# Optimization experiments

Hardware: AMD Instinct MI355X
Metric: run time of the kernel (lower is better)

Reference implementation:

```python
import jax, jax.numpy as jnp
import numpy as np


def _maxpool2x2(t):
    # t: [B, H, W, C] -> [B, H//2, W//2, C], 2x2 max pool stride 2
    B, H, W, C = t.shape
    return t.reshape(B, H // 2, 2, W // 2, 2, C).max(axis=(2, 4))


def setup_inputs() -> dict:
    key = jax.random.key(0)
    ks = jax.random.split(key, 7)
    B, H, W, C = 16, 64, 64, 256
    x = jax.random.normal(ks[0], (B, H, W, C), jnp.float32)
    w_theta = jax.random.normal(ks[1], (C, C // 8), jnp.float32) * 0.05
    w_phi = jax.random.normal(ks[2], (C, C // 8), jnp.float32) * 0.05
    w_g = jax.random.normal(ks[3], (C, C // 2), jnp.float32) * 0.05
    w_o = jax.random.normal(ks[4], (C // 2, C), jnp.float32) * 0.05
    b_o = jnp.zeros((C,), jnp.float32)
    sigma = jax.random.normal(ks[5], (), jnp.float32)
    return {"x": x, "w_theta": w_theta, "w_phi": w_phi, "w_g": w_g,
            "w_o": w_o, "b_o": b_o, "sigma": sigma}


def reference(x, w_theta, w_phi, w_g, w_o, b_o, sigma):
    B, H, W, C = x.shape
    L = H * W          # location_num = 4096
    Ld = L // 4        # downsampled_num (after 2x2 maxpool)
    # 1x1 convs == channel GEMMs
    theta = jnp.einsum('bhwc,cd->bhwd', x, w_theta).reshape(B, L, C // 8)
    phi = jnp.einsum('bhwc,cd->bhwd', x, w_phi)
    phi = _maxpool2x2(phi).reshape(B, Ld, C // 8)
    attn = jax.nn.softmax(jnp.einsum('bld,bmd->blm', theta, phi), axis=-1)  # [B, L, Ld]
    g = jnp.einsum('bhwc,cd->bhwd', x, w_g)
    g = _maxpool2x2(g).reshape(B, Ld, C // 2)
    attn_g = jnp.einsum('blm,bmd->bld', attn, g).reshape(B, H, W, C // 2)
    attn_g = jnp.einsum('bhwd,dc->bhwc', attn_g, w_o) + b_o
    return x + sigma * attn_g
```

## Files before the change

### kernel.cpp

```cpp
#include <hip/hip_runtime.h>
#include <hip/hip_bf16.h>


typedef __attribute__((ext_vector_type(8))) short bf16x8;
typedef __attribute__((ext_vector_type(4))) float f32x4;

#define MFMA16(A,B,C) __builtin_amdgcn_mfma_f32_16x16x32_bf16(A,B,C,0,0,0)

#define GLOAD16(GSRC, LDST)                                                        \
    __builtin_amdgcn_global_load_lds(                                              \
        (const __attribute__((address_space(1))) unsigned int*)(GSRC),             \
        (__attribute__((address_space(3))) unsigned int*)(LDST), 16, 0, 0)

static __device__ __forceinline__ unsigned short f2b(float f) {
    __hip_bfloat16 h = __float2bfloat16(f);
    return *reinterpret_cast<unsigned short*>(&h);
}
static __device__ __forceinline__ float blo(unsigned int u){ return __uint_as_float(u << 16); }
static __device__ __forceinline__ float bhi(unsigned int u){ return __uint_as_float(u & 0xffff0000u); }

__global__ void k_prep(const float* __restrict__ w_theta, const float* __restrict__ w_phi,
                       const float* __restrict__ w_g, const float* __restrict__ w_o,
                       unsigned short* __restrict__ WT, unsigned short* __restrict__ woT)
{
    int bid = blockIdx.x, t = threadIdx.x;
    if (bid < 192) {
        int n = bid;
        float v;
        if (n < 32)      v = w_theta[t * 32 + n];
        else if (n < 64) v = w_phi[t * 32 + (n - 32)];
        else             v = w_g[t * 128 + (n - 64)];
        WT[n * 256 + t] = f2b(v);
    } else if (t < 128) {
        int cc = bid - 192;
        woT[cc * 128 + t] = f2b(w_o[t * 256 + cc]);
    }
}

__global__ __launch_bounds__(256) void k_proj(
    const float* __restrict__ x, const unsigned short* __restrict__ WT,
    unsigned short* __restrict__ theta_b, unsigned short* __restrict__ phi_b,
    unsigned short* __restrict__ g_b)
{
    __shared__ unsigned short xT[128 * 64];
    __shared__ unsigned short wT[192 * 64];
    const int t = threadIdx.x;
    const int w = t >> 6, l = t & 63, G = l >> 4, c = l & 15;
    const size_t row0 = (size_t)blockIdx.x * 128;

    f32x4 acc[2][12];
#pragma unroll
    for (int i = 0; i < 2; i++)
#pragma unroll
        for (int j = 0; j < 12; j++) acc[i][j] = (f32x4){0.f, 0.f, 0.f, 0.f};

    for (int k0 = 0; k0 < 256; k0 += 64) {
        __syncthreads();
#pragma unroll
        for (int it = 0; it < 4; it++) {
            int u = it * 256 + t, r = u >> 3, s = u & 7;
            const float* px = x + (row0 + r) * 256 + k0 + s * 8;
            float4 a = *(const float4*)px;
            float4 bq = *(const float4*)(px + 4);
            uint4 v;
            v.x = (unsigned)f2b(a.x) | ((unsigned)f2b(a.y) << 16);
            v.y = (unsigned)f2b(a.z) | ((unsigned)f2b(a.w) << 16);
            v.z = (unsigned)f2b(bq.x) | ((unsigned)f2b(bq.y) << 16);
            v.w = (unsigned)f2b(bq.z) | ((unsigned)f2b(bq.w) << 16);
            *(uint4*)((char*)xT + r * 128 + ((s * 16) ^ ((r & 7) << 4))) = v;
        }
#pragma unroll
        for (int it = 0; it < 6; it++) {
            int u = it * 256 + t, r = u >> 3, s = u & 7;
            uint4 v = *(const uint4*)(WT + r * 256 + k0 + s * 8);
            *(uint4*)((char*)wT + r * 128 + ((s * 16) ^ ((r & 7) << 4))) = v;
        }
        __syncthreads();
#pragma unroll
        for (int kin = 0; kin < 2; kin++) {
            int m0r = (2 * w) * 16 + c, m1r = (2 * w + 1) * 16 + c;
            bf16x8 a0 = *(const bf16x8*)((char*)xT + m0r * 128 + ((kin * 64 + G * 16) ^ ((m0r & 7) << 4)));
            bf16x8 a1 = *(const bf16x8*)((char*)xT + m1r * 128 + ((kin * 64 + G * 16) ^ ((m1r & 7) << 4)));
#pragma unroll
            for (int nt = 0; nt < 12; nt++) {
                int nr = nt * 16 + c;
                bf16x8 bv = *(const bf16x8*)((char*)wT + nr * 128 + ((kin * 64 + G * 16) ^ ((nr & 7) << 4)));
                acc[0][nt] = MFMA16(a0, bv, acc[0][nt]);
                acc[1][nt] = MFMA16(a1, bv, acc[1][nt]);
            }
        }
    }
#pragma unroll
    for (int mt = 0; mt < 2; mt++)
#pragma unroll
        for (int nt = 0; nt < 12; nt++)
#pragma unroll
            for (int i = 0; i < 4; i++) {
                size_t row = row0 + (2 * w + mt) * 16 + 4 * G + i;
                unsigned short v = f2b(acc[mt][nt][i]);
                if (nt < 2)      theta_b[row * 32 + nt * 16 + c] = v;
                else if (nt < 4) phi_b[row * 32 + (nt - 2) * 16 + c] = v;
                else             g_b[row * 128 + (nt - 4) * 16 + c] = v;
            }
}

__global__ __launch_bounds__(256) void k_pool(
    const unsigned short* __restrict__ phi_b, const unsigned short* __restrict__ g_b,
    unsigned short* __restrict__ phi_p, unsigned short* __restrict__ g_pT)
{
    const int bid = blockIdx.x, t = threadIdx.x;
    if (bid < 1024) {
        const unsigned int* p32 = (const unsigned int*)phi_b;
        unsigned int* pp32 = (unsigned int*)phi_p;
        int idx = bid * 256 + t;
        int b = idx >> 14, r = idx & 16383, pm = r >> 4, d2 = r & 15;
        int hp = pm >> 5, wp = pm & 31;
        size_t base = ((size_t)b * 4096 + (2 * hp) * 64 + 2 * wp) * 16 + d2;
        unsigned v0 = p32[base], v1 = p32[base + 16], v2 = p32[base + 1024], v3 = p32[base + 1040];
        float lo = fmaxf(fmaxf(blo(v0), blo(v1)), fmaxf(blo(v2), blo(v3)));
        float hi = fmaxf(fmaxf(bhi(v0), bhi(v1)), fmaxf(bhi(v2), bhi(v3)));
        pp32[idx] = (unsigned)f2b(lo) | ((unsigned)f2b(hi) << 16);
    } else {
        __shared__ unsigned short P[32 * 128];
        int b = (bid - 1024) >> 5, hp = (bid - 1024) & 31;
        const unsigned int* g32 = (const unsigned int*)g_b;
#pragma unroll
        for (int it = 0; it < 8; it++) {
            int u = it * 256 + t, wp = u >> 6, d2 = u & 63;
            size_t base = ((size_t)b * 4096 + (2 * hp) * 64 + 2 * wp) * 64 + d2;
            unsigned v0 = g32[base], v1 = g32[base + 64], v2 = g32[base + 4096], v3 = g32[base + 4160];
            float lo = fmaxf(fmaxf(blo(v0), blo(v1)), fmaxf(blo(v2), blo(v3)));
            float hi = fmaxf(fmaxf(bhi(v0), bhi(v1)), fmaxf(bhi(v2), bhi(v3)));
            unsigned pv = (unsigned)f2b(lo) | ((unsigned)f2b(hi) << 16);
            *(unsigned*)((char*)P + wp * 256 + ((d2 * 4) ^ ((wp & 7) << 4))) = pv;
        }
        __syncthreads();
#pragma unroll
        for (int it = 0; it < 2; it++) {
            int d = t & 127, s4 = (t >> 7) + it * 2;
            union { unsigned short v[8]; uint4 q; } pk;
#pragma unroll
            for (int k = 0; k < 8; k++) {
                int wp = 16 * (k >> 2) + 4 * s4 + (k & 3);
                pk.v[k] = *(const unsigned short*)((char*)P + wp * 256 + ((d * 2) ^ ((wp & 7) << 4)));
            }
            *(uint4*)(g_pT + ((size_t)b * 128 + d) * 1024 + hp * 32 + s4 * 8) = pk.q;
        }
    }
}

__global__ __launch_bounds__(256, 4) void k_attn(
    const unsigned short* __restrict__ theta_b, const unsigned short* __restrict__ phi_p,
    const unsigned short* __restrict__ g_pT, const unsigned short* __restrict__ woT,
    const float* __restrict__ x, const float* __restrict__ b_o,
    const float* __restrict__ sigma_p, float* __restrict__ out)
{
    __shared__ char lds[40960];

    const int t = threadIdx.x;
    const int w = t >> 6, l = t & 63, G = l >> 4, c = l & 15;
    const int qg = w >> 1, mg = w & 1;
    const int bid = (blockIdx.x & 7) * 128 + (blockIdx.x >> 3);
    const int b = bid >> 6;
    const int q0 = (bid & 63) * 64;
    const int xr = (c & 7) << 4;

    const unsigned short* gsrc = g_pT + (size_t)b * 131072;
    const unsigned short* psrc = phi_p + (size_t)b * 32768;
#define STAGE(BI, MC)                                                               \
    {                                                                               \
        char* gb = lds + mg * 20480 + (BI) * 10240;                                 \
        char* pb = gb + 8192;                                                       \
        const int hp = mg * 16 + (MC);                                              \
        _Pragma("unroll")                                                           \
        for (int it = 0; it < 4; it++) {                                            \
            int d = 64 * qg + 16 * it + (l >> 2);                                   \
            GLOAD16(gsrc + (size_t)d * 1024 + hp * 32 + (l & 3) * 8,                \
                    gb + qg * 4096 + it * 1024 + l * 16);                           \
        }                                                                           \
        {                                                                           \
            int r = 16 * qg + (l >> 2);                                             \
            GLOAD16(psrc + (size_t)(hp * 32 + r) * 32 + (l & 3) * 8,                \
                    pb + qg * 1024 + l * 16);                                       \
        }                                                                           \
    }

    STAGE(0, 0);
    {
        char* th = lds + 10240;
        int r = t >> 2, s = t & 3;
        uint4 v = *(const uint4*)(theta_b + ((size_t)(b * 4096 + q0 + r)) * 32 + s * 8);
        *(uint4*)(th + r * 64 + s * 16) = v;
    }
    __syncthreads();

    const bf16x8 bt0 = *(const bf16x8*)(lds + 10240 + (qg * 32 + c) * 64 + G * 16);
    const bf16x8 bt1 = *(const bf16x8*)(lds + 10240 + (qg * 32 + 16 + c) * 64 + G * 16);
    __syncthreads();

    f32x4 oacc[2][8];
#pragma unroll
    for (int qt = 0; qt < 2; qt++)
#pragma unroll
        for (int dt = 0; dt < 8; dt++) oacc[qt][dt] = (f32x4){0.f, 0.f, 0.f, 0.f};
    float ps[2] = {0.f, 0.f};
    const f32x4 zf = (f32x4){0.f, 0.f, 0.f, 0.f};

    for (int mc = 0; mc < 16; mc++) {
        const int cur = mc & 1;
        if (mc < 15) {
            STAGE(cur ^ 1, mc + 1);
            asm volatile("s_waitcnt vmcnt(5)" ::: "memory");
        } else {
            asm volatile("s_waitcnt vmcnt(0)" ::: "memory");
        }
        __builtin_amdgcn_sched_barrier(0);
        __builtin_amdgcn_s_barrier();
        __builtin_amdgcn_sched_barrier(0);

        const char* gL   = lds + mg * 20480 + cur * 10240;
        const char* phiL = gL + 8192;

        bf16x8 ap0 = *(const bf16x8*)(phiL + c * 64 + G * 16);
        bf16x8 ap1 = *(const bf16x8*)(phiL + (16 + c) * 64 + G * 16);
        f32x4 sacc[2][2];
        __builtin_amdgcn_s_setprio(1);
        sacc[0][0] = MFMA16(ap0, bt0, zf);
        sacc[0][1] = MFMA16(ap1, bt0, zf);
        sacc[1][0] = MFMA16(ap0, bt1, zf);
        sacc[1][1] = MFMA16(ap1, bt1, zf);
        __builtin_amdgcn_s_setprio(0);

        bf16x8 pa[2];
#pragma unroll
        for (int qt = 0; qt < 2; qt++) {
            union { unsigned u[4]; bf16x8 v; } pu;
#pragma unroll
            for (int mt = 0; mt < 2; mt++)
#pragma unroll
                for (int hf = 0; hf < 2; hf++) {
                    float p0 = __expf(sacc[qt][mt][2 * hf]);
                    float p1 = __expf(sacc[qt][mt][2 * hf + 1]);
                    ps[qt] += p0 + p1;
                    pu.u[mt * 2 + hf] = (unsigned)f2b(p0) | ((unsigned)f2b(p1) << 16);
                }
            pa[qt] = pu.v;
        }

        __builtin_amdgcn_s_setprio(1);
#pragma unroll
        for (int dt = 0; dt < 8; dt++) {
            bf16x8 bg = *(const bf16x8*)(gL + (dt * 16 + c) * 64 + G * 16);
            oacc[0][dt] = MFMA16(pa[0], bg, oacc[0][dt]);
            oacc[1][dt] = MFMA16(pa[1], bg, oacc[1][dt]);
        }
        __builtin_amdgcn_s_setprio(0);

        asm volatile("s_waitcnt lgkmcnt(0)" ::: "memory");
        __builtin_amdgcn_sched_barrier(0);
        __builtin_amdgcn_s_barrier();
        __builtin_amdgcn_sched_barrier(0);
    }
#undef STAGE

#pragma unroll
    for (int qt = 0; qt < 2; qt++) {
        ps[qt] += __shfl_xor(ps[qt], 16);
        ps[qt] += __shfl_xor(ps[qt], 32);
    }

    if (mg == 1) {
        char* po = lds + qg * 16640;
#pragma unroll
        for (int qt = 0; qt < 2; qt++)
#pragma unroll
            for (int dt = 0; dt < 8; dt++)
#pragma unroll
                for (int i = 0; i < 4; i++)
                    *(float*)(po + (qt * 16 + 4 * G + i) * 520 + (dt * 16 + c) * 4) =
                        oacc[qt][dt][i];
        if (l < 16) {
            *(float*)(lds + 33280 + (qg * 32 + l) * 4)      = ps[0];
            *(float*)(lds + 33280 + (qg * 32 + 16 + l) * 4) = ps[1];
        }
    }
    __syncthreads();
    if (mg == 0) {
        const char* po = lds + qg * 16640;
#pragma unroll
        for (int qt = 0; qt < 2; qt++)
#pragma unroll
            for (int dt = 0; dt < 8; dt++) {
                f32x4 a = oacc[qt][dt];
#pragma unroll
                for (int i = 0; i < 4; i++)
                    a[i] += *(const float*)(po + (qt * 16 + 4 * G + i) * 520 + (dt * 16 + c) * 4);
                oacc[qt][dt] = a;
            }
#pragma unroll
        for (int qt = 0; qt < 2; qt++)
            ps[qt] += *(const float*)(lds + 33280 + (qg * 32 + qt * 16 + c) * 4);
        float rinv[2][4];
#pragma unroll
        for (int qt = 0; qt < 2; qt++)
#pragma unroll
            for (int i = 0; i < 4; i++)
                rinv[qt][i] = 1.0f / __shfl(ps[qt], 4 * G + i);
        char* Or = lds + qg * 16640;
#pragma unroll
        for (int qt = 0; qt < 2; qt++)
#pragma unroll
            for (int dt = 0; dt < 8; dt++)
#pragma unroll
                for (int i = 0; i < 4; i++) {
                    int r32 = qt * 16 + 4 * G + i, d = dt * 16 + c;
                    *(unsigned short*)(Or + r32 * 256 + ((d * 2) ^ ((r32 & 7) << 4))) =
                        f2b(oacc[qt][dt][i] * rinv[qt][i]);
                }
    }
    __syncthreads();

    const float sg = *sigma_p;
    const char* O_r = lds + (w >> 1) * 16640 + ((w & 1) * 16 + c) * 256;
    char* wo_l = lds + 8448;
    bf16x8 aO[4];
#pragma unroll
    for (int ks = 0; ks < 4; ks++)
        aO[ks] = *(const bf16x8*)(O_r + ((ks * 64 + G * 16) ^ xr));

    for (int cb = 0; cb < 8; cb++) {
        __syncthreads();
#pragma unroll
        for (int it = 0; it < 2; it++) {
            int u = it * 256 + t, r = u >> 4, s = u & 15;
            uint4 v = *(const uint4*)(woT + (size_t)(cb * 32 + r) * 128 + s * 8);
            *(uint4*)(wo_l + r * 256 + ((s * 16) ^ ((r & 7) << 4))) = v;
        }
        __syncthreads();
        f32x4 eacc[2];
#pragma unroll
        for (int ct = 0; ct < 2; ct++) eacc[ct] = (f32x4){0.f, 0.f, 0.f, 0.f};
#pragma unroll
        for (int ks = 0; ks < 4; ks++) {
#pragma unroll
            for (int ct = 0; ct < 2; ct++) {
                bf16x8 bw = *(const bf16x8*)(wo_l + (ct * 16 + c) * 256 + ((ks * 64 + G * 16) ^ xr));
                eacc[ct] = MFMA16(aO[ks], bw, eacc[ct]);
            }
        }
#pragma unroll
        for (int ct = 0; ct < 2; ct++) {
            int col = cb * 32 + ct * 16 + c;
            float bo = b_o[col];
#pragma unroll
            for (int i = 0; i < 4; i++) {
                size_t off = ((size_t)(b * 4096 + q0 + w * 16 + 4 * G + i)) * 256 + col;
                out[off] = x[off] + sg * (eacc[ct][i] + bo);
            }
        }
    }
}

extern "C" void kernel_launch(void* const* d_in, const int* in_sizes, int n_in,
                              void* d_out, int out_size, void* d_ws, size_t ws_size,
                              hipStream_t stream)
{
    const float* x       = (const float*)d_in[0];
    const float* w_theta = (const float*)d_in[1];
    const float* w_phi   = (const float*)d_in[2];
    const float* w_g     = (const float*)d_in[3];
    const float* w_o     = (const float*)d_in[4];
    const float* b_o     = (const float*)d_in[5];
    const float* sigma   = (const float*)d_in[6];
    float* out = (float*)d_out;

    char* ws = (char*)d_ws;
    unsigned short* theta_b = (unsigned short*)(ws);
    unsigned short* phi_b   = (unsigned short*)(ws + 4194304);
    unsigned short* g_b     = (unsigned short*)(ws + 8388608);
    unsigned short* phi_p   = (unsigned short*)(ws + 25165824);
    unsigned short* g_pT    = (unsigned short*)(ws + 26214400);
    unsigned short* WT      = (unsigned short*)(ws + 30408704);
    unsigned short* woT     = (unsigned short*)(ws + 30507008);

    hipLaunchKernelGGL(k_prep, dim3(448), dim3(256), 0, stream,
                       w_theta, w_phi, w_g, w_o, WT, woT);
    hipLaunchKernelGGL(k_proj, dim3(512), dim3(256), 0, stream,
                       x, WT, theta_b, phi_b, g_b);
    hipLaunchKernelGGL(k_pool, dim3(1536), dim3(256), 0, stream,
                       phi_b, g_b, phi_p, g_pT);
    hipLaunchKernelGGL(k_attn, dim3(1024), dim3(256), 0, stream,
                       theta_b, phi_p, g_pT, woT, x, b_o, sigma, out);
}
```

Measured before the change: 77.46 us.

## Fuse 2x2 max-pool into projection kernel, use exp2 softmax, restructure attention pipeline

The max-pool and transpose of phi and g now run inside the projection kernel's epilogue through LDS, which removes the separate pool kernel and the full-resolution phi/g round trip through global memory. Each 128-row block covers two image rows, so the pool is done in registers and then across rows in LDS. Theta weights are pre-scaled by log2(e) so the softmax can use the hardware exp2 instruction. The attention loop now has one barrier per iteration, with the next stage's load issued after a full vmcnt(0) wait, which may reduce load/compute overlap.

```diff
diff --git a/kernel.cpp b/kernel.cpp
--- a/kernel.cpp
+++ b/kernel.cpp
@@ -16,8 +16,12 @@
     __hip_bfloat16 h = __float2bfloat16(f);
     return *reinterpret_cast<unsigned short*>(&h);
 }
-static __device__ __forceinline__ float blo(unsigned int u){ return __uint_as_float(u << 16); }
-static __device__ __forceinline__ float bhi(unsigned int u){ return __uint_as_float(u & 0xffff0000u); }
+static __device__ __forceinline__ unsigned short bmax(unsigned short a, unsigned short b) {
+    return (__uint_as_float((unsigned)a << 16) > __uint_as_float((unsigned)b << 16)) ? a : b;
+}
+static __device__ __forceinline__ float fexp2(float f) {
+    return __builtin_amdgcn_exp2f(f);
+}
 
 __global__ void k_prep(const float* __restrict__ w_theta, const float* __restrict__ w_phi,
                        const float* __restrict__ w_g, const float* __restrict__ w_o,
@@ -27,7 +31,7 @@
     if (bid < 192) {
         int n = bid;
         float v;
-        if (n < 32)      v = w_theta[t * 32 + n];
+        if (n < 32)      v = w_theta[t * 32 + n] * 1.44269504f;
         else if (n < 64) v = w_phi[t * 32 + (n - 32)];
         else             v = w_g[t * 128 + (n - 64)];
         WT[n * 256 + t] = f2b(v);
@@ -39,14 +43,18 @@
 
 __global__ __launch_bounds__(256) void k_proj(
     const float* __restrict__ x, const unsigned short* __restrict__ WT,
-    unsigned short* __restrict__ theta_b, unsigned short* __restrict__ phi_b,
-    unsigned short* __restrict__ g_b)
+    unsigned short* __restrict__ theta_b, unsigned short* __restrict__ phi_p,
+    unsigned short* __restrict__ g_pT)
 {
-    __shared__ unsigned short xT[128 * 64];
-    __shared__ unsigned short wT[192 * 64];
+    __shared__ char plds[40960];
+    unsigned short* xT = (unsigned short*)plds;
+    unsigned short* wT = (unsigned short*)(plds + 16384);
+
     const int t = threadIdx.x;
     const int w = t >> 6, l = t & 63, G = l >> 4, c = l & 15;
-    const size_t row0 = (size_t)blockIdx.x * 128;
+    const int bid = blockIdx.x;
+    const int b = bid >> 5, h2 = bid & 31;
+    const size_t row0 = (size_t)bid * 128;
 
     f32x4 acc[2][12];
 #pragma unroll
@@ -90,62 +98,63 @@
             }
         }
     }
+
 #pragma unroll
     for (int mt = 0; mt < 2; mt++)
 #pragma unroll
-        for (int nt = 0; nt < 12; nt++)
+        for (int nt = 0; nt < 2; nt++)
 #pragma unroll
             for (int i = 0; i < 4; i++) {
                 size_t row = row0 + (2 * w + mt) * 16 + 4 * G + i;
-                unsigned short v = f2b(acc[mt][nt][i]);
-                if (nt < 2)      theta_b[row * 32 + nt * 16 + c] = v;
-                else if (nt < 4) phi_b[row * 32 + (nt - 2) * 16 + c] = v;
-                else             g_b[row * 128 + (nt - 4) * 16 + c] = v;
-            }
-}
-
-__global__ __launch_bounds__(256) void k_pool(
-    const unsigned short* __restrict__ phi_b, const unsigned short* __restrict__ g_b,
-    unsigned short* __restrict__ phi_p, unsigned short* __restrict__ g_pT)
-{
-    const int bid = blockIdx.x, t = threadIdx.x;
-    if (bid < 1024) {
-        const unsigned int* p32 = (const unsigned int*)phi_b;
-        unsigned int* pp32 = (unsigned int*)phi_p;
-        int idx = bid * 256 + t;
-        int b = idx >> 14, r = idx & 16383, pm = r >> 4, d2 = r & 15;
-        int hp = pm >> 5, wp = pm & 31;
-        size_t base = ((size_t)b * 4096 + (2 * hp) * 64 + 2 * wp) * 16 + d2;
-        unsigned v0 = p32[base], v1 = p32[base + 16], v2 = p32[base + 1024], v3 = p32[base + 1040];
-        float lo = fmaxf(fmaxf(blo(v0), blo(v1)), fmaxf(blo(v2), blo(v3)));
-        float hi = fmaxf(fmaxf(bhi(v0), bhi(v1)), fmaxf(bhi(v2), bhi(v3)));
-        pp32[idx] = (unsigned)f2b(lo) | ((unsigned)f2b(hi) << 16);
-    } else {
-        __shared__ unsigned short P[32 * 128];
-        int b = (bid - 1024) >> 5, hp = (bid - 1024) & 31;
-        const unsigned int* g32 = (const unsigned int*)g_b;
-#pragma unroll
-        for (int it = 0; it < 8; it++) {
-            int u = it * 256 + t, wp = u >> 6, d2 = u & 63;
-            size_t base = ((size_t)b * 4096 + (2 * hp) * 64 + 2 * wp) * 64 + d2;
-            unsigned v0 = g32[base], v1 = g32[base + 64], v2 = g32[base + 4096], v3 = g32[base + 4160];
-            float lo = fmaxf(fmaxf(blo(v0), blo(v1)), fmaxf(blo(v2), blo(v3)));
-            float hi = fmaxf(fmaxf(bhi(v0), bhi(v1)), fmaxf(bhi(v2), bhi(v3)));
-            unsigned pv = (unsigned)f2b(lo) | ((unsigned)f2b(hi) << 16);
-            *(unsigned*)((char*)P + wp * 256 + ((d2 * 4) ^ ((wp & 7) << 4))) = pv;
-        }
-        __syncthreads();
-#pragma unroll
-        for (int it = 0; it < 2; it++) {
-            int d = t & 127, s4 = (t >> 7) + it * 2;
-            union { unsigned short v[8]; uint4 q; } pk;
-#pragma unroll
-            for (int k = 0; k < 8; k++) {
-                int wp = 16 * (k >> 2) + 4 * s4 + (k & 3);
-                pk.v[k] = *(const unsigned short*)((char*)P + wp * 256 + ((d * 2) ^ ((wp & 7) << 4)));
-            }
-            *(uint4*)(g_pT + ((size_t)b * 128 + d) * 1024 + hp * 32 + s4 * 8) = pk.q;
-        }
+                theta_b[row * 32 + nt * 16 + c] = f2b(acc[mt][nt][i]);
+            }
+
+    __syncthreads();
+
+#pragma unroll
+    for (int mt = 0; mt < 2; mt++) {
+        int rl = 2 * w + mt, rr = rl >> 2, wpb = (rl & 3) * 8 + 2 * G;
+#pragma unroll
+        for (int nt = 2; nt < 12; nt++) {
+            int col = (nt - 2) * 16 + c;
+#pragma unroll
+            for (int j = 0; j < 2; j++) {
+                int row = rr * 32 + wpb + j;
+                float m = fmaxf(acc[mt][nt][2 * j], acc[mt][nt][2 * j + 1]);
+                *(unsigned short*)(plds + row * 512 + ((2 * col) ^ ((row & 7) << 4))) = f2b(m);
+            }
+        }
+    }
+    __syncthreads();
+
+    {
+        int wp = t >> 3, chb = (t & 7) * 4;
+        unsigned short vv[4];
+#pragma unroll
+        for (int k = 0; k < 4; k++) {
+            int colb = 2 * (chb + k);
+            unsigned short a = *(const unsigned short*)(plds + wp * 512 + (colb ^ ((wp & 7) << 4)));
+            unsigned short e = *(const unsigned short*)(plds + (wp + 32) * 512 + (colb ^ ((wp & 7) << 4)));
+            vv[k] = bmax(a, e);
+        }
+        uint2 pv;
+        pv.x = (unsigned)vv[0] | ((unsigned)vv[1] << 16);
+        pv.y = (unsigned)vv[2] | ((unsigned)vv[3] << 16);
+        *(uint2*)(phi_p + ((size_t)(b * 1024 + h2 * 32 + wp)) * 32 + chb) = pv;
+    }
+#pragma unroll
+    for (int it = 0; it < 2; it++) {
+        int d = t & 127, s4 = (t >> 7) + 2 * it;
+        union { unsigned short v[8]; uint4 q; } pk;
+#pragma unroll
+        for (int k = 0; k < 8; k++) {
+            int wp2 = 16 * (k >> 2) + 4 * s4 + (k & 3);
+            int colb = 2 * (32 + d);
+            unsigned short a = *(const unsigned short*)(plds + wp2 * 512 + (colb ^ ((wp2 & 7) << 4)));
+            unsigned short e = *(const unsigned short*)(plds + (wp2 + 32) * 512 + (colb ^ ((wp2 & 7) << 4)));
+            pk.v[k] = bmax(a, e);
+        }
+        *(uint4*)(g_pT + ((size_t)b * 128 + d) * 1024 + h2 * 32 + s4 * 8) = pk.q;
     }
 }
 
@@ -208,15 +217,11 @@
 
     for (int mc = 0; mc < 16; mc++) {
         const int cur = mc & 1;
-        if (mc < 15) {
-            STAGE(cur ^ 1, mc + 1);
-            asm volatile("s_waitcnt vmcnt(5)" ::: "memory");
-        } else {
-            asm volatile("s_waitcnt vmcnt(0)" ::: "memory");
-        }
+        asm volatile("s_waitcnt vmcnt(0)" ::: "memory");
         __builtin_amdgcn_sched_barrier(0);
         __builtin_amdgcn_s_barrier();
         __builtin_amdgcn_sched_barrier(0);
+        if (mc < 15) STAGE(cur ^ 1, mc + 1);
 
         const char* gL   = lds + mg * 20480 + cur * 10240;
         const char* phiL = gL + 8192;
@@ -239,8 +244,8 @@
             for (int mt = 0; mt < 2; mt++)
 #pragma unroll
                 for (int hf = 0; hf < 2; hf++) {
-                    float p0 = __expf(sacc[qt][mt][2 * hf]);
-                    float p1 = __expf(sacc[qt][mt][2 * hf + 1]);
+                    float p0 = fexp2(sacc[qt][mt][2 * hf]);
+                    float p1 = fexp2(sacc[qt][mt][2 * hf + 1]);
                     ps[qt] += p0 + p1;
                     pu.u[mt * 2 + hf] = (unsigned)f2b(p0) | ((unsigned)f2b(p1) << 16);
                 }
@@ -255,13 +260,9 @@
             oacc[1][dt] = MFMA16(pa[1], bg, oacc[1][dt]);
         }
         __builtin_amdgcn_s_setprio(0);
-
-        asm volatile("s_waitcnt lgkmcnt(0)" ::: "memory");
-        __builtin_amdgcn_sched_barrier(0);
-        __builtin_amdgcn_s_barrier();
-        __builtin_amdgcn_sched_barrier(0);
     }
 #undef STAGE
+    __syncthreads();
 
 #pragma unroll
     for (int qt = 0; qt < 2; qt++) {
@@ -376,19 +377,15 @@
 
     char* ws = (char*)d_ws;
     unsigned short* theta_b = (unsigned short*)(ws);
-    unsigned short* phi_b   = (unsigned short*)(ws + 4194304);
-    unsigned short* g_b     = (unsigned short*)(ws + 8388608);
-    unsigned short* phi_p   = (unsigned short*)(ws + 25165824);
-    unsigned short* g_pT    = (unsigned short*)(ws + 26214400);
-    unsigned short* WT      = (unsigned short*)(ws + 30408704);
-    unsigned short* woT     = (unsigned short*)(ws + 30507008);
+    unsigned short* phi_p   = (unsigned short*)(ws + 4194304);
+    unsigned short* g_pT    = (unsigned short*)(ws + 5242880);
+    unsigned short* WT      = (unsigned short*)(ws + 9437184);
+    unsigned short* woT     = (unsigned short*)(ws + 9535488);
 
     hipLaunchKernelGGL(k_prep, dim3(448), dim3(256), 0, stream,
                        w_theta, w_phi, w_g, w_o, WT, woT);
     hipLaunchKernelGGL(k_proj, dim3(512), dim3(256), 0, stream,
-                       x, WT, theta_b, phi_b, g_b);
-    hipLaunchKernelGGL(k_pool, dim3(1536), dim3(256), 0, stream,
-                       phi_b, g_b, phi_p, g_pT);
+                       x, WT, theta_b, phi_p, g_pT);
     hipLaunchKernelGGL(k_attn, dim3(1024), dim3(256), 0, stream,
                        theta_b, phi_p, g_pT, woT, x, b_o, sigma, out);
 }
```

New measurement: 69.76 us. 1.11x faster.
